# Optimization experiments

Hardware: AMD Instinct MI355X
Metric: run time of the kernel (lower is better)

## Reference

```python
import jax, jax.numpy as jnp
import numpy as np

B, H, S, D = 4, 16, 2048, 128
HIDDEN_DIM = 128  # init arg; used as softmax scale


def setup_inputs() -> dict:
    key = jax.random.key(0)
    kq, kk, kv = jax.random.split(key, 3)
    q = jax.random.normal(kq, (B, H, S, D), dtype=jnp.float32)
    k = jax.random.normal(kk, (B, H, S, D), dtype=jnp.float32)
    v = jax.random.normal(kv, (B, H, S, D), dtype=jnp.float32)
    return {"q": q, "k": k, "v": v}


def reference(q, k, v):
    # scores[b,h,s,t] = sum_d q[b,h,s,d] * k[b,h,t,d]  (y permuted on last two dims, then matmul)
    scores = jnp.einsum("bhsd,bhtd->bhst", q, k) * (HIDDEN_DIM ** -0.5)
    probs = jax.nn.softmax(scores, axis=-1)
    return jnp.einsum("bhst,bhtd->bhsd", probs, v)
```

## Files before the change

### kernel.cpp

```cpp
#include <hip/hip_runtime.h>
#include <hip/hip_bf16.h>


#define SEQ 2048
#define DH  128
#define NBH 64
#define BM  64
#define BN  64
#define NT  (SEQ / BN)
#define QK_LD 136
#define VT_LD 72
#define P_LD  72
#define THR 8.0f

typedef __attribute__((ext_vector_type(8))) short short8;
typedef __attribute__((ext_vector_type(4))) float f32x4;

#if __has_builtin(__builtin_amdgcn_exp2f)
#define EXP2F(x) __builtin_amdgcn_exp2f(x)
#else
#define EXP2F(x) exp2f(x)
#endif

#define CS (0.08838834764831845f * 1.44269504088896340736f)

__device__ __forceinline__ unsigned int pk_bf16(float lo, float hi) {
    union { __hip_bfloat162 h; unsigned int u; } cv;
    cv.h = __float22bfloat162_rn(make_float2(lo, hi));
    return cv.u;
}

template<bool DOK>
__global__ __launch_bounds__(256) void prep_kernel(
        const float* __restrict__ v, unsigned short* __restrict__ vt,
        const float* __restrict__ k, unsigned short* __restrict__ kb) {
    __shared__ float tile[64][65];
    const int bh = blockIdx.z;
    const int s0 = blockIdx.x * 64;
    const int d0 = blockIdx.y * 64;
    const int tid = threadIdx.x;

    if (DOK) {
        const size_t kbase = ((size_t)blockIdx.x +
                              32 * ((size_t)blockIdx.y + 2 * (size_t)blockIdx.z)) * 4096;
#pragma unroll
        for (int i = 0; i < 4; ++i) {
            size_t idx = kbase + ((size_t)tid + 256 * i) * 4;
            float4 val = *reinterpret_cast<const float4*>(k + idx);
            uint2 pk;
            pk.x = pk_bf16(val.x, val.y);
            pk.y = pk_bf16(val.z, val.w);
            *reinterpret_cast<uint2*>(kb + idx) = pk;
        }
    }

    const float* src = v + ((size_t)bh * SEQ + s0) * DH + d0;
#pragma unroll
    for (int i = 0; i < 4; ++i) {
        int id  = tid + 256 * i;
        int row = id >> 4;
        int c4  = (id & 15) << 2;
        float4 val = *reinterpret_cast<const float4*>(src + row * DH + c4);
        tile[row][c4 + 0] = val.x;
        tile[row][c4 + 1] = val.y;
        tile[row][c4 + 2] = val.z;
        tile[row][c4 + 3] = val.w;
    }
    __syncthreads();
    unsigned short* dst = vt + ((size_t)bh * DH + d0) * SEQ + s0;
#pragma unroll
    for (int i = 0; i < 2; ++i) {
        int id = tid + 256 * i;
        int dd = id >> 3;
        int kc = (id & 7) << 3;
        uint4 pk;
        unsigned int* pw = reinterpret_cast<unsigned int*>(&pk);
#pragma unroll
        for (int j = 0; j < 4; ++j)
            pw[j] = pk_bf16(tile[kc + 2 * j][dd], tile[kc + 2 * j + 1][dd]);
        *reinterpret_cast<uint4*>(dst + (size_t)dd * SEQ + kc) = pk;
    }
}

template<bool KPRE>
__global__ __launch_bounds__(256, 3) void fattn_kernel(
        const float* __restrict__ q, const float* __restrict__ kf,
        const unsigned short* __restrict__ kb,
        const unsigned short* __restrict__ vt, float* __restrict__ out) {
    __shared__ unsigned short Ks[BN * QK_LD];
    __shared__ unsigned short Vs[DH * VT_LD];
    __shared__ unsigned short Ps[BM * P_LD];

    const int wid = ((blockIdx.x & 7) << 8) | (blockIdx.x >> 3);
    const int bh  = wid >> 5;
    const int q0  = (wid & 31) * BM;
    const int tid  = threadIdx.x;
    const int w    = tid >> 6;
    const int lane = tid & 63;
    const int l15  = lane & 15;
    const int quad = lane >> 4;

    short8 qf[4];
    {
        const float* qptr = q + ((size_t)bh * SEQ + q0 + w * 16 + l15) * DH + quad * 8;
#pragma unroll
        for (int kk = 0; kk < 4; ++kk) {
            float4 x = *reinterpret_cast<const float4*>(qptr + kk * 32);
            float4 y = *reinterpret_cast<const float4*>(qptr + kk * 32 + 4);
            union { short8 s; uint4 u; } cv;
            cv.u.x = pk_bf16(x.x * CS, x.y * CS);
            cv.u.y = pk_bf16(x.z * CS, x.w * CS);
            cv.u.z = pk_bf16(y.x * CS, y.y * CS);
            cv.u.w = pk_bf16(y.z * CS, y.w * CS);
            qf[kk] = cv.s;
        }
    }

    f32x4 o[8];
#pragma unroll
    for (int t = 0; t < 8; ++t) o[t] = (f32x4){0.f, 0.f, 0.f, 0.f};
    float mrow[4] = {-1e30f, -1e30f, -1e30f, -1e30f};
    float lrow[4] = {0.f, 0.f, 0.f, 0.f};

    const float*          kfp  = kf + (size_t)bh * SEQ * DH;
    const unsigned short* kbp  = kb + (size_t)bh * SEQ * DH;
    const unsigned short* vptr = vt + (size_t)bh * DH * SEQ;

    unsigned int* Ps32 = reinterpret_cast<unsigned int*>(Ps);
    const int prow_base = w * 16 + quad * 4;
    const int pdw = (l15 & 1) ? (8 + (l15 >> 1)) : (l15 >> 1);

    uint4 kr0, kr1, kr2, kr3, vr0, vr1, vr2, vr3;
    const int krow = tid >> 4, kcol = (tid & 15) << 3;
    const int vrow = tid >> 3, vcol = (tid & 7) << 3;
    const unsigned short* kst = kbp + (size_t)krow * DH + kcol;
    const unsigned short* vst = vptr + (size_t)vrow * SEQ + vcol;

#define LOAD_TILE(K0)                                                              \
    do {                                                                           \
        const unsigned short* _kp = kst + (size_t)(K0) * DH;                       \
        kr0 = *reinterpret_cast<const uint4*>(_kp);                                \
        kr1 = *reinterpret_cast<const uint4*>(_kp + 16 * DH);                      \
        kr2 = *reinterpret_cast<const uint4*>(_kp + 32 * DH);                      \
        kr3 = *reinterpret_cast<const uint4*>(_kp + 48 * DH);                      \
        const unsigned short* _vp = vst + (K0);                                    \
        vr0 = *reinterpret_cast<const uint4*>(_vp);                                \
        vr1 = *reinterpret_cast<const uint4*>(_vp + 32 * SEQ);                     \
        vr2 = *reinterpret_cast<const uint4*>(_vp + 64 * SEQ);                     \
        vr3 = *reinterpret_cast<const uint4*>(_vp + 96 * SEQ);                     \
    } while (0)

#define WRITE_TILE()                                                               \
    do {                                                                           \
        *reinterpret_cast<uint4*>(&Ks[(krow     ) * QK_LD + kcol]) = kr0;          \
        *reinterpret_cast<uint4*>(&Ks[(krow + 16) * QK_LD + kcol]) = kr1;          \
        *reinterpret_cast<uint4*>(&Ks[(krow + 32) * QK_LD + kcol]) = kr2;          \
        *reinterpret_cast<uint4*>(&Ks[(krow + 48) * QK_LD + kcol]) = kr3;          \
        *reinterpret_cast<uint4*>(&Vs[(vrow     ) * VT_LD + vcol]) = vr0;          \
        *reinterpret_cast<uint4*>(&Vs[(vrow + 32) * VT_LD + vcol]) = vr1;          \
        *reinterpret_cast<uint4*>(&Vs[(vrow + 64) * VT_LD + vcol]) = vr2;          \
        *reinterpret_cast<uint4*>(&Vs[(vrow + 96) * VT_LD + vcol]) = vr3;          \
    } while (0)

    if (KPRE) {
        LOAD_TILE(0);
        WRITE_TILE();
        __syncthreads();
    }

    for (int kt = 0; kt < NT; ++kt) {
        const int k0 = kt * BN;
        if (KPRE) {
            if (kt + 1 < NT) LOAD_TILE(k0 + BN);
        } else {
#pragma unroll
            for (int i = 0; i < 8; ++i) {
                int id  = tid + 256 * i;
                int row = id >> 5;
                int c4  = (id & 31) << 2;
                float4 val = *reinterpret_cast<const float4*>(kfp + (size_t)(k0 + row) * DH + c4);
                uint2 pk;
                pk.x = pk_bf16(val.x, val.y);
                pk.y = pk_bf16(val.z, val.w);
                *reinterpret_cast<uint2*>(&Ks[row * QK_LD + c4]) = pk;
            }
#pragma unroll
            for (int i = 0; i < 4; ++i) {
                int id = tid + 256 * i;
                int dd = id >> 3;
                int kc = (id & 7) << 3;
                *reinterpret_cast<uint4*>(&Vs[dd * VT_LD + kc]) =
                    *reinterpret_cast<const uint4*>(vptr + (size_t)dd * SEQ + k0 + kc);
            }
            __syncthreads();
        }

        f32x4 acc[4];
#pragma unroll
        for (int t = 0; t < 4; ++t) acc[t] = (f32x4){0.f, 0.f, 0.f, 0.f};
#pragma unroll
        for (int kk = 0; kk < 4; ++kk) {
            const int koff = kk * 32 + quad * 8;
#pragma unroll
            for (int t = 0; t < 4; ++t) {
                short8 b = *reinterpret_cast<const short8*>(&Ks[(t * 16 + l15) * QK_LD + koff]);
                acc[t] = __builtin_amdgcn_mfma_f32_16x16x32_bf16(qf[kk], b, acc[t], 0, 0, 0);
            }
        }

        float lm[4];
#pragma unroll
        for (int r = 0; r < 4; ++r)
            lm[r] = fmaxf(fmaxf(acc[0][r], acc[1][r]), fmaxf(acc[2][r], acc[3][r]));
        float need = fmaxf(fmaxf(lm[0] - mrow[0], lm[1] - mrow[1]),
                           fmaxf(lm[2] - mrow[2], lm[3] - mrow[3]));
        if (__any(need > THR)) {
#pragma unroll
            for (int r = 0; r < 4; ++r) {
                float mx = lm[r];
#pragma unroll
                for (int off = 1; off < 16; off <<= 1)
                    mx = fmaxf(mx, __shfl_xor(mx, off));
                float mnew  = fmaxf(mrow[r], mx);
                float alpha = EXP2F(mrow[r] - mnew);
                mrow[r] = mnew;
                lrow[r] *= alpha;
#pragma unroll
                for (int t = 0; t < 8; ++t) o[t][r] *= alpha;
            }
        }

#pragma unroll
        for (int r = 0; r < 4; ++r) {
            float p0 = EXP2F(acc[0][r] - mrow[r]);
            float p1 = EXP2F(acc[1][r] - mrow[r]);
            float p2 = EXP2F(acc[2][r] - mrow[r]);
            float p3 = EXP2F(acc[3][r] - mrow[r]);
            lrow[r] += (p0 + p1) + (p2 + p3);
            unsigned int a01 = pk_bf16(p0, p1);
            unsigned int a23 = pk_bf16(p2, p3);
            unsigned int s01 = __shfl_xor((int)a01, 1);
            unsigned int s23 = __shfl_xor((int)a23, 1);
            unsigned int w0, w1;
            if (l15 & 1) {
                w0 = (s01 >> 16) | (a01 & 0xffff0000u);
                w1 = (s23 >> 16) | (a23 & 0xffff0000u);
            } else {
                w0 = (a01 & 0xffffu) | (s01 << 16);
                w1 = (a23 & 0xffffu) | (s23 << 16);
            }
            const int dw = (prow_base + r) * (P_LD / 2) + pdw;
            Ps32[dw]      = w0;
            Ps32[dw + 16] = w1;
        }

#pragma unroll
        for (int kk = 0; kk < 2; ++kk) {
            const int koff = kk * 32 + quad * 8;
            short8 a = *reinterpret_cast<const short8*>(&Ps[(w * 16 + l15) * P_LD + koff]);
#pragma unroll
            for (int t = 0; t < 8; ++t) {
                short8 b = *reinterpret_cast<const short8*>(&Vs[(t * 16 + l15) * VT_LD + koff]);
                o[t] = __builtin_amdgcn_mfma_f32_16x16x32_bf16(a, b, o[t], 0, 0, 0);
            }
        }
        __syncthreads();
        if (KPRE) {
            if (kt + 1 < NT) WRITE_TILE();
            __syncthreads();
        }
    }

#pragma unroll
    for (int r = 0; r < 4; ++r) {
#pragma unroll
        for (int off = 1; off < 16; off <<= 1)
            lrow[r] += __shfl_xor(lrow[r], off);
    }
    float* obase = out + ((size_t)bh * SEQ + q0) * DH;
#pragma unroll
    for (int r = 0; r < 4; ++r) {
        float inv = 1.0f / lrow[r];
        int row = w * 16 + quad * 4 + r;
#pragma unroll
        for (int t = 0; t < 8; ++t)
            obase[(size_t)row * DH + t * 16 + l15] = o[t][r] * inv;
    }
}

extern "C" void kernel_launch(void* const* d_in, const int* in_sizes, int n_in,
                              void* d_out, int out_size, void* d_ws, size_t ws_size,
                              hipStream_t stream) {
    const float* q = (const float*)d_in[0];
    const float* k = (const float*)d_in[1];
    const float* v = (const float*)d_in[2];
    float* out = (float*)d_out;
    unsigned short* vt = (unsigned short*)d_ws;

    const size_t vt_elems = (size_t)NBH * SEQ * DH;
    if (ws_size >= 2 * vt_elems * sizeof(unsigned short)) {
        unsigned short* kbuf = vt + vt_elems;
        prep_kernel<true><<<dim3(SEQ / 64, DH / 64, NBH), dim3(256), 0, stream>>>(v, vt, k, kbuf);
        fattn_kernel<true><<<dim3(SEQ / BM * NBH), dim3(256), 0, stream>>>(q, nullptr, kbuf, vt, out);
    } else {
        prep_kernel<false><<<dim3(SEQ / 64, DH / 64, NBH), dim3(256), 0, stream>>>(v, vt, nullptr, nullptr);
        fattn_kernel<false><<<dim3(SEQ / BM * NBH), dim3(256), 0, stream>>>(q, k, nullptr, vt, out);
    }
}
```

Baseline: 419.9 us.

## Rework attention kernel around 32x32x16 MFMA with register-resident probabilities

```diff
diff --git a/kernel.cpp b/kernel.cpp
--- a/kernel.cpp
+++ b/kernel.cpp
@@ -5,7 +5,7 @@
 #define SEQ 2048
 #define DH  128
 #define NBH 64
-#define BM  64
+#define BM  128
 #define BN  64
 #define NT  (SEQ / BN)
 #define QK_LD 136
@@ -15,6 +15,7 @@
 
 typedef __attribute__((ext_vector_type(8))) short short8;
 typedef __attribute__((ext_vector_type(4))) float f32x4;
+typedef __attribute__((ext_vector_type(16))) float f32x16;
 
 #if __has_builtin(__builtin_amdgcn_exp2f)
 #define EXP2F(x) __builtin_amdgcn_exp2f(x)
@@ -34,17 +35,15 @@
 __global__ __launch_bounds__(256) void prep_kernel(
         const float* __restrict__ v, unsigned short* __restrict__ vt,
         const float* __restrict__ k, unsigned short* __restrict__ kb) {
-    __shared__ float tile[64][65];
-    const int bh = blockIdx.z;
-    const int s0 = blockIdx.x * 64;
-    const int d0 = blockIdx.y * 64;
+    __shared__ float tile[64][129];
+    const int bh  = blockIdx.z;
+    const int s0  = blockIdx.x * 64;
     const int tid = threadIdx.x;
 
     if (DOK) {
-        const size_t kbase = ((size_t)blockIdx.x +
-                              32 * ((size_t)blockIdx.y + 2 * (size_t)blockIdx.z)) * 4096;
-#pragma unroll
-        for (int i = 0; i < 4; ++i) {
+        const size_t kbase = ((size_t)blockIdx.x + 32 * (size_t)bh) * 8192;
+#pragma unroll
+        for (int i = 0; i < 8; ++i) {
             size_t idx = kbase + ((size_t)tid + 256 * i) * 4;
             float4 val = *reinterpret_cast<const float4*>(k + idx);
             uint2 pk;
@@ -54,12 +53,12 @@
         }
     }
 
-    const float* src = v + ((size_t)bh * SEQ + s0) * DH + d0;
-#pragma unroll
-    for (int i = 0; i < 4; ++i) {
+    const float* src = v + ((size_t)bh * SEQ + s0) * DH;
+#pragma unroll
+    for (int i = 0; i < 8; ++i) {
         int id  = tid + 256 * i;
-        int row = id >> 4;
-        int c4  = (id & 15) << 2;
+        int row = id >> 5;
+        int c4  = (id & 31) << 2;
         float4 val = *reinterpret_cast<const float4*>(src + row * DH + c4);
         tile[row][c4 + 0] = val.x;
         tile[row][c4 + 1] = val.y;
@@ -67,9 +66,9 @@
         tile[row][c4 + 3] = val.w;
     }
     __syncthreads();
-    unsigned short* dst = vt + ((size_t)bh * DH + d0) * SEQ + s0;
-#pragma unroll
-    for (int i = 0; i < 2; ++i) {
+    unsigned short* dst = vt + (size_t)bh * DH * SEQ + s0;
+#pragma unroll
+    for (int i = 0; i < 4; ++i) {
         int id = tid + 256 * i;
         int dd = id >> 3;
         int kc = (id & 7) << 3;
@@ -82,53 +81,44 @@
     }
 }
 
-template<bool KPRE>
-__global__ __launch_bounds__(256, 3) void fattn_kernel(
-        const float* __restrict__ q, const float* __restrict__ kf,
-        const unsigned short* __restrict__ kb,
+__global__ __launch_bounds__(256, 2) void fattn_kernel(
+        const float* __restrict__ q, const unsigned short* __restrict__ kb,
         const unsigned short* __restrict__ vt, float* __restrict__ out) {
     __shared__ unsigned short Ks[BN * QK_LD];
     __shared__ unsigned short Vs[DH * VT_LD];
-    __shared__ unsigned short Ps[BM * P_LD];
-
-    const int wid = ((blockIdx.x & 7) << 8) | (blockIdx.x >> 3);
-    const int bh  = wid >> 5;
-    const int q0  = (wid & 31) * BM;
+
+    const int wid = ((blockIdx.x & 7) << 7) | (blockIdx.x >> 3);
+    const int bh  = wid >> 4;
+    const int q0  = (wid & 15) * BM;
     const int tid  = threadIdx.x;
     const int w    = tid >> 6;
     const int lane = tid & 63;
-    const int l15  = lane & 15;
-    const int quad = lane >> 4;
-
-    short8 qf[4];
+    const int l31  = lane & 31;
+    const int hi   = lane >> 5;
+
+    short8 qb[8];
     {
-        const float* qptr = q + ((size_t)bh * SEQ + q0 + w * 16 + l15) * DH + quad * 8;
-#pragma unroll
-        for (int kk = 0; kk < 4; ++kk) {
-            float4 x = *reinterpret_cast<const float4*>(qptr + kk * 32);
-            float4 y = *reinterpret_cast<const float4*>(qptr + kk * 32 + 4);
+        const float* qptr = q + ((size_t)bh * SEQ + q0 + w * 32 + l31) * DH + hi * 8;
+#pragma unroll
+        for (int ks = 0; ks < 8; ++ks) {
+            float4 x = *reinterpret_cast<const float4*>(qptr + 16 * ks);
+            float4 y = *reinterpret_cast<const float4*>(qptr + 16 * ks + 4);
             union { short8 s; uint4 u; } cv;
             cv.u.x = pk_bf16(x.x * CS, x.y * CS);
             cv.u.y = pk_bf16(x.z * CS, x.w * CS);
             cv.u.z = pk_bf16(y.x * CS, y.y * CS);
             cv.u.w = pk_bf16(y.z * CS, y.w * CS);
-            qf[kk] = cv.s;
-        }
-    }
-
-    f32x4 o[8];
-#pragma unroll
-    for (int t = 0; t < 8; ++t) o[t] = (f32x4){0.f, 0.f, 0.f, 0.f};
-    float mrow[4] = {-1e30f, -1e30f, -1e30f, -1e30f};
-    float lrow[4] = {0.f, 0.f, 0.f, 0.f};
-
-    const float*          kfp  = kf + (size_t)bh * SEQ * DH;
+            qb[ks] = cv.s;
+        }
+    }
+
+    f32x16 o0, o1, o2, o3;
+#pragma unroll
+    for (int i = 0; i < 16; ++i) { o0[i] = 0.f; o1[i] = 0.f; o2[i] = 0.f; o3[i] = 0.f; }
+    float m = -1e30f, lsum = 0.f;
+
     const unsigned short* kbp  = kb + (size_t)bh * SEQ * DH;
     const unsigned short* vptr = vt + (size_t)bh * DH * SEQ;
-
-    unsigned int* Ps32 = reinterpret_cast<unsigned int*>(Ps);
-    const int prow_base = w * 16 + quad * 4;
-    const int pdw = (l15 & 1) ? (8 + (l15 >> 1)) : (l15 >> 1);
 
     uint4 kr0, kr1, kr2, kr3, vr0, vr1, vr2, vr3;
     const int krow = tid >> 4, kcol = (tid & 15) << 3;
@@ -162,38 +152,177 @@
         *reinterpret_cast<uint4*>(&Vs[(vrow + 96) * VT_LD + vcol]) = vr3;          \
     } while (0)
 
-    if (KPRE) {
-        LOAD_TILE(0);
-        WRITE_TILE();
+    LOAD_TILE(0);
+    WRITE_TILE();
+    __syncthreads();
+
+    const unsigned short* KsA = &Ks[l31 * QK_LD + hi * 8];
+    const unsigned short* VsA = &Vs[l31 * VT_LD + hi * 8];
+
+    for (int kt = 0; kt < NT; ++kt) {
+        f32x16 s0, s1;
+#pragma unroll
+        for (int i = 0; i < 16; ++i) { s0[i] = 0.f; s1[i] = 0.f; }
+        __builtin_amdgcn_s_setprio(1);
+#pragma unroll
+        for (int ks = 0; ks < 8; ++ks) {
+            short8 a0 = *reinterpret_cast<const short8*>(KsA + 16 * ks);
+            short8 a1 = *reinterpret_cast<const short8*>(KsA + 32 * QK_LD + 16 * ks);
+            s0 = __builtin_amdgcn_mfma_f32_32x32x16_bf16(a0, qb[ks], s0, 0, 0, 0);
+            s1 = __builtin_amdgcn_mfma_f32_32x32x16_bf16(a1, qb[ks], s1, 0, 0, 0);
+        }
+        __builtin_amdgcn_s_setprio(0);
+
+        float mx = s0[0];
+#pragma unroll
+        for (int i = 1; i < 16; ++i) mx = fmaxf(mx, s0[i]);
+#pragma unroll
+        for (int i = 0; i < 16; ++i) mx = fmaxf(mx, s1[i]);
+        mx = fmaxf(mx, __shfl_xor(mx, 32));
+        if (__any(mx - m > THR)) {
+            float mn = fmaxf(m, mx);
+            float al = EXP2F(m - mn);
+            m = mn; lsum *= al;
+#pragma unroll
+            for (int i = 0; i < 16; ++i) { o0[i] *= al; o1[i] *= al; o2[i] *= al; o3[i] *= al; }
+        }
+#pragma unroll
+        for (int i = 0; i < 16; ++i) s0[i] = EXP2F(s0[i] - m);
+#pragma unroll
+        for (int i = 0; i < 16; ++i) s1[i] = EXP2F(s1[i] - m);
+        float ls = 0.f;
+#pragma unroll
+        for (int i = 0; i < 16; ++i) ls += s0[i] + s1[i];
+        lsum += ls;
+
+        short8 pf0, pf1, pf2, pf3;
+#define MAKE_PF(PF, SG, S)                                                         \
+        {                                                                          \
+            unsigned pq0 = pk_bf16(SG[8*(S)+0], SG[8*(S)+1]);                      \
+            unsigned pq1 = pk_bf16(SG[8*(S)+2], SG[8*(S)+3]);                      \
+            unsigned pq2 = pk_bf16(SG[8*(S)+4], SG[8*(S)+5]);                      \
+            unsigned pq3 = pk_bf16(SG[8*(S)+6], SG[8*(S)+7]);                      \
+            unsigned px0 = (unsigned)__shfl_xor((int)pq0, 32);                     \
+            unsigned px1 = (unsigned)__shfl_xor((int)pq1, 32);                     \
+            unsigned px2 = (unsigned)__shfl_xor((int)pq2, 32);                     \
+            unsigned px3 = (unsigned)__shfl_xor((int)pq3, 32);                     \
+            union { short8 s; uint4 u; } cv;                                       \
+            cv.u.x = hi ? px2 : pq0;                                               \
+            cv.u.y = hi ? px3 : pq1;                                               \
+            cv.u.z = hi ? pq2 : px0;                                               \
+            cv.u.w = hi ? pq3 : px1;                                               \
+            PF = cv.s;                                                             \
+        }
+        MAKE_PF(pf0, s0, 0)
+        MAKE_PF(pf1, s0, 1)
+        MAKE_PF(pf2, s1, 0)
+        MAKE_PF(pf3, s1, 1)
+
+        if (kt + 1 < NT) LOAD_TILE((kt + 1) * BN);
+
+        __builtin_amdgcn_s_setprio(1);
+#define PV_C(OC, C)                                                                \
+        {                                                                          \
+            short8 va0 = *reinterpret_cast<const short8*>(VsA + (32*(C)) * VT_LD);      \
+            short8 va1 = *reinterpret_cast<const short8*>(VsA + (32*(C)) * VT_LD + 16); \
+            short8 va2 = *reinterpret_cast<const short8*>(VsA + (32*(C)) * VT_LD + 32); \
+            short8 va3 = *reinterpret_cast<const short8*>(VsA + (32*(C)) * VT_LD + 48); \
+            OC = __builtin_amdgcn_mfma_f32_32x32x16_bf16(va0, pf0, OC, 0, 0, 0);   \
+            OC = __builtin_amdgcn_mfma_f32_32x32x16_bf16(va1, pf1, OC, 0, 0, 0);   \
+            OC = __builtin_amdgcn_mfma_f32_32x32x16_bf16(va2, pf2, OC, 0, 0, 0);   \
+            OC = __builtin_amdgcn_mfma_f32_32x32x16_bf16(va3, pf3, OC, 0, 0, 0);   \
+        }
+        PV_C(o0, 0) PV_C(o1, 1) PV_C(o2, 2) PV_C(o3, 3)
+        __builtin_amdgcn_s_setprio(0);
+
         __syncthreads();
-    }
+        if (kt + 1 < NT) WRITE_TILE();
+        __syncthreads();
+    }
+
+    lsum += __shfl_xor(lsum, 32);
+    float inv = 1.0f / lsum;
+    float* obase = out + ((size_t)bh * SEQ + q0 + w * 32 + l31) * DH + 4 * hi;
+#define STORE_C(OC, C)                                                             \
+    {                                                                              \
+        _Pragma("unroll")                                                          \
+        for (int u = 0; u < 4; ++u) {                                              \
+            float4 st;                                                             \
+            st.x = OC[4*u+0] * inv; st.y = OC[4*u+1] * inv;                        \
+            st.z = OC[4*u+2] * inv; st.w = OC[4*u+3] * inv;                        \
+            *reinterpret_cast<float4*>(obase + 32*(C) + 8*u) = st;                 \
+        }                                                                          \
+    }
+    STORE_C(o0, 0) STORE_C(o1, 1) STORE_C(o2, 2) STORE_C(o3, 3)
+}
+
+__global__ __launch_bounds__(256, 3) void fattn_fallback(
+        const float* __restrict__ q, const float* __restrict__ kf,
+        const unsigned short* __restrict__ vt, float* __restrict__ out) {
+    __shared__ unsigned short Ks[64 * QK_LD];
+    __shared__ unsigned short Vs[DH * VT_LD];
+    __shared__ unsigned short Ps[64 * P_LD];
+
+    const int wid = ((blockIdx.x & 7) << 8) | (blockIdx.x >> 3);
+    const int bh  = wid >> 5;
+    const int q0  = (wid & 31) * 64;
+    const int tid  = threadIdx.x;
+    const int w    = tid >> 6;
+    const int lane = tid & 63;
+    const int l15  = lane & 15;
+    const int quad = lane >> 4;
+
+    short8 qf[4];
+    {
+        const float* qptr = q + ((size_t)bh * SEQ + q0 + w * 16 + l15) * DH + quad * 8;
+#pragma unroll
+        for (int kk = 0; kk < 4; ++kk) {
+            float4 x = *reinterpret_cast<const float4*>(qptr + kk * 32);
+            float4 y = *reinterpret_cast<const float4*>(qptr + kk * 32 + 4);
+            union { short8 s; uint4 u; } cv;
+            cv.u.x = pk_bf16(x.x * CS, x.y * CS);
+            cv.u.y = pk_bf16(x.z * CS, x.w * CS);
+            cv.u.z = pk_bf16(y.x * CS, y.y * CS);
+            cv.u.w = pk_bf16(y.z * CS, y.w * CS);
+            qf[kk] = cv.s;
+        }
+    }
+
+    f32x4 o[8];
+#pragma unroll
+    for (int t = 0; t < 8; ++t) o[t] = (f32x4){0.f, 0.f, 0.f, 0.f};
+    float mrow[4] = {-1e30f, -1e30f, -1e30f, -1e30f};
+    float lrow[4] = {0.f, 0.f, 0.f, 0.f};
+
+    const float*          kfp  = kf + (size_t)bh * SEQ * DH;
+    const unsigned short* vptr = vt + (size_t)bh * DH * SEQ;
+
+    unsigned int* Ps32 = reinterpret_cast<unsigned int*>(Ps);
+    const int prow_base = w * 16 + quad * 4;
+    const int pdw = (l15 & 1) ? (8 + (l15 >> 1)) : (l15 >> 1);
 
     for (int kt = 0; kt < NT; ++kt) {
         const int k0 = kt * BN;
-        if (KPRE) {
-            if (kt + 1 < NT) LOAD_TILE(k0 + BN);
-        } else {
-#pragma unroll
-            for (int i = 0; i < 8; ++i) {
-                int id  = tid + 256 * i;
-                int row = id >> 5;
-                int c4  = (id & 31) << 2;
-                float4 val = *reinterpret_cast<const float4*>(kfp + (size_t)(k0 + row) * DH + c4);
-                uint2 pk;
-                pk.x = pk_bf16(val.x, val.y);
-                pk.y = pk_bf16(val.z, val.w);
-                *reinterpret_cast<uint2*>(&Ks[row * QK_LD + c4]) = pk;
-            }
-#pragma unroll
-            for (int i = 0; i < 4; ++i) {
-                int id = tid + 256 * i;
-                int dd = id >> 3;
-                int kc = (id & 7) << 3;
-                *reinterpret_cast<uint4*>(&Vs[dd * VT_LD + kc]) =
-                    *reinterpret_cast<const uint4*>(vptr + (size_t)dd * SEQ + k0 + kc);
-            }
-            __syncthreads();
-        }
+#pragma unroll
+        for (int i = 0; i < 8; ++i) {
+            int id  = tid + 256 * i;
+            int row = id >> 5;
+            int c4  = (id & 31) << 2;
+            float4 val = *reinterpret_cast<const float4*>(kfp + (size_t)(k0 + row) * DH + c4);
+            uint2 pk;
+            pk.x = pk_bf16(val.x, val.y);
+            pk.y = pk_bf16(val.z, val.w);
+            *reinterpret_cast<uint2*>(&Ks[row * QK_LD + c4]) = pk;
+        }
+#pragma unroll
+        for (int i = 0; i < 4; ++i) {
+            int id = tid + 256 * i;
+            int dd = id >> 3;
+            int kc = (id & 7) << 3;
+            *reinterpret_cast<uint4*>(&Vs[dd * VT_LD + kc]) =
+                *reinterpret_cast<const uint4*>(vptr + (size_t)dd * SEQ + k0 + kc);
+        }
+        __syncthreads();
 
         f32x4 acc[4];
 #pragma unroll
@@ -265,10 +394,6 @@
             }
         }
         __syncthreads();
-        if (KPRE) {
-            if (kt + 1 < NT) WRITE_TILE();
-            __syncthreads();
-        }
     }
 
 #pragma unroll
@@ -300,10 +425,10 @@
     const size_t vt_elems = (size_t)NBH * SEQ * DH;
     if (ws_size >= 2 * vt_elems * sizeof(unsigned short)) {
         unsigned short* kbuf = vt + vt_elems;
-        prep_kernel<true><<<dim3(SEQ / 64, DH / 64, NBH), dim3(256), 0, stream>>>(v, vt, k, kbuf);
-        fattn_kernel<true><<<dim3(SEQ / BM * NBH), dim3(256), 0, stream>>>(q, nullptr, kbuf, vt, out);
+        prep_kernel<true><<<dim3(SEQ / 64, 1, NBH), dim3(256), 0, stream>>>(v, vt, k, kbuf);
+        fattn_kernel<<<dim3((SEQ / BM) * NBH), dim3(256), 0, stream>>>(q, kbuf, vt, out);
     } else {
-        prep_kernel<false><<<dim3(SEQ / 64, DH / 64, NBH), dim3(256), 0, stream>>>(v, vt, nullptr, nullptr);
-        fattn_kernel<false><<<dim3(SEQ / BM * NBH), dim3(256), 0, stream>>>(q, k, nullptr, vt, out);
+        prep_kernel<false><<<dim3(SEQ / 64, 1, NBH), dim3(256), 0, stream>>>(v, vt, nullptr, nullptr);
+        fattn_fallback<<<dim3((SEQ / 64) * NBH), dim3(256), 0, stream>>>(q, k, vt, out);
     }
 }
```

Measured after the change: 364.4 us. 13.2% less time.
